# Optimization experiments

Hardware: AMD Instinct MI355X
Metric: run time of the kernel (lower is better)

The kernel has to match this reference:

```python
import jax, jax.numpy as jnp
import numpy as np

D = 1024        # embed_size
F = 4096        # ffn_dim
E = 8           # n_experts
K = 2           # top_k_experts
NS = 1          # n_shared
T = 8192        # tokens


def setup_inputs() -> dict:
    key = jax.random.key(0)
    ks = jax.random.split(key, 12)
    s = lambda *sh: 1.0 / np.sqrt(sh[-2] if len(sh) > 1 else sh[-1])
    inp = {
        "x": jax.random.normal(ks[0], (T, D), jnp.float32),
        "gate_w": jax.random.normal(ks[1], (D, E), jnp.float32) * (1.0 / np.sqrt(D)),
        "gate_b": jnp.zeros((E,), jnp.float32),
        "shared_w1": jax.random.normal(ks[2], (NS, D, 2 * F), jnp.float32) * (1.0 / np.sqrt(D)),
        "shared_b1": jnp.zeros((NS, 2 * F), jnp.float32),
        "shared_w2": jax.random.normal(ks[3], (NS, F, D), jnp.float32) * (1.0 / np.sqrt(F)),
        "shared_b2": jnp.zeros((NS, D), jnp.float32),
        "routed_w1": jax.random.normal(ks[4], (E, D, 2 * F), jnp.float32) * (1.0 / np.sqrt(D)),
        "routed_b1": jnp.zeros((E, 2 * F), jnp.float32),
        "routed_w2": jax.random.normal(ks[5], (E, F, D), jnp.float32) * (1.0 / np.sqrt(F)),
        "routed_b2": jnp.zeros((E, D), jnp.float32),
    }
    return inp


def _expert(x, w1, b1, w2, b2):
    # SwiGLU FFN: w2( silu(a) * b ) where [a, b] = chunk(x @ w1 + b1)
    h = x @ w1 + b1                      # [T, 2F]
    a, b = jnp.split(h, 2, axis=-1)      # [T, F] each
    return (jax.nn.silu(a) * b) @ w2 + b2  # [T, D]


def reference(x, gate_w, gate_b, shared_w1, shared_b1, shared_w2, shared_b2,
              routed_w1, routed_b1, routed_w2, routed_b2):
    # shared experts (always active)
    shared_out = jnp.zeros_like(x)
    for i in range(NS):
        shared_out = shared_out + _expert(x, shared_w1[i], shared_b1[i], shared_w2[i], shared_b2[i])

    # softmax gating + top-k selection
    logits = x @ gate_w + gate_b                      # [T, E]
    probs = jax.nn.softmax(logits, axis=-1)
    topk_probs, topk_idx = jax.lax.top_k(probs, K)    # [T, K]

    # per-token combine weight for each expert: sum_k p_k * 1[idx_k == e]
    one_hot = jax.nn.one_hot(topk_idx, E, dtype=x.dtype)        # [T, K, E]
    combine = jnp.einsum("tk,tke->te", topk_probs, one_hot)     # [T, E]

    # dispatch/combine: dense per-expert FFN, weighted by combine (zero off-route)
    routed_out = jnp.zeros_like(x)
    for e in range(E):
        y = _expert(x, routed_w1[e], routed_b1[e], routed_w2[e], routed_b2[e])
        routed_out = routed_out + y * combine[:, e:e + 1]

    return shared_out + routed_out
```

## Files before the change

kernel.cpp:

```cpp
#include <hip/hip_runtime.h>

#define TOK   8192
#define DD    1024
#define FF    4096
#define EE    8
#define TWOF  8192
#define NSLOT 16384
#define PADT  17408

typedef unsigned short u16;
typedef float  f32x16 __attribute__((ext_vector_type(16)));
typedef __bf16 bf16x8 __attribute__((ext_vector_type(8)));

__device__ __forceinline__ u16 f2b(float f) {
  unsigned u = __builtin_bit_cast(unsigned, f);
  u += 0x7fffu + ((u >> 16) & 1u);
  return (u16)(u >> 16);
}

__device__ __forceinline__ void ldslds16(const void* g, void* l) {
  __builtin_amdgcn_global_load_lds((const __attribute__((address_space(1))) void*)g,
                                   (__attribute__((address_space(3))) void*)l, 16, 0, 0);
}

__global__ void gate_kernel(const float* __restrict__ x, const float* __restrict__ gw,
                            const float* __restrict__ gb, int* __restrict__ counts,
                            int* __restrict__ eidx, int* __restrict__ epos,
                            float* __restrict__ ew) {
  const int wave = threadIdx.x >> 6, lane = threadIdx.x & 63;
  const int t = blockIdx.x * 4 + wave;
  float acc[EE] = {0,0,0,0,0,0,0,0};
  const float* xr = x + (size_t)t * DD;
  for (int d = lane; d < DD; d += 64) {
    float xv = xr[d];
    const float* g = gw + (size_t)d * EE;
#pragma unroll
    for (int e = 0; e < EE; ++e) acc[e] += xv * g[e];
  }
#pragma unroll
  for (int e = 0; e < EE; ++e)
#pragma unroll
    for (int off = 32; off > 0; off >>= 1) acc[e] += __shfl_down(acc[e], off);
  if (lane == 0) {
    float l[EE];
#pragma unroll
    for (int e = 0; e < EE; ++e) l[e] = acc[e] + gb[e];
    int i0 = 0;
    for (int e = 1; e < EE; ++e) if (l[e] > l[i0]) i0 = e;
    int i1 = (i0 == 0) ? 1 : 0;
    for (int e = 0; e < EE; ++e) { if (e == i0) continue; if (l[e] > l[i1]) i1 = e; }
    float m = l[0];
    for (int e = 1; e < EE; ++e) m = fmaxf(m, l[e]);
    float s = 0.f, p[EE];
    for (int e = 0; e < EE; ++e) { p[e] = __expf(l[e] - m); s += p[e]; }
    float w0 = p[i0] / s, w1 = p[i1] / s;
    int p0 = atomicAdd(&counts[i0], 1);
    int p1 = atomicAdd(&counts[i1], 1);
    eidx[2*t] = i0; eidx[2*t+1] = i1;
    epos[2*t] = p0; epos[2*t+1] = p1;
    ew[2*t] = w0;  ew[2*t+1] = w1;
  }
}

__global__ void setup_kernel(const int* __restrict__ counts, int* __restrict__ meta) {
  if (threadIdx.x == 0 && blockIdx.x == 0) {
    int s = 0, tm = 0;
    for (int e = 0; e < EE; ++e) {
      meta[e] = s;
      meta[8 + e] = tm;
      s  += (counts[e] + 127) & ~127;
      tm += (counts[e] + 127) >> 7;
    }
    meta[16] = tm;
  }
}

__global__ void slot_kernel(const int* __restrict__ eidx, const int* __restrict__ epos,
                            const float* __restrict__ ew, const int* __restrict__ meta,
                            int* __restrict__ s2t, float* __restrict__ swt,
                            int* __restrict__ t2s) {
  int i = blockIdx.x * 256 + threadIdx.x;
  int e = eidx[i];
  int slot = meta[e] + epos[i];
  s2t[slot] = i >> 1;
  swt[slot] = ew[i];
  t2s[i] = slot;
}

__global__ void cvtx_kernel(const float* __restrict__ x, u16* __restrict__ xb) {
  int i = blockIdx.x * 256 + threadIdx.x;
  float4 v = ((const float4*)x)[i];
  unsigned lo = (unsigned)f2b(v.x) | ((unsigned)f2b(v.y) << 16);
  unsigned hi = (unsigned)f2b(v.z) | ((unsigned)f2b(v.w) << 16);
  ((uint2*)xb)[i] = make_uint2(lo, hi);
}

__global__ void gather_kernel(const u16* __restrict__ xb, const int* __restrict__ s2t,
                              u16* __restrict__ xg) {
  int i = blockIdx.x * 256 + threadIdx.x;
  int row = i >> 7, c = i & 127;
  int tok = s2t[row];
  ((int4*)xg)[(size_t)row * 128 + c] = ((const int4*)xb)[(size_t)tok * 128 + c];
}

__global__ void wt_kernel(const float* __restrict__ srcS, const float* __restrict__ srcR,
                          u16* __restrict__ dst, int K, int N, int permute) {
  __shared__ float tile[32][33];
  const int seg = blockIdx.z;
  const float* src = (seg == 0) ? srcS : srcR + (size_t)(seg - 1) * K * N;
  const int pc0 = blockIdx.x * 32, k0 = blockIdx.y * 32;
  const int tid = threadIdx.x;
  {
    int kk = tid >> 3, j4 = (tid & 7) << 2;
    const float* srow = src + (size_t)(k0 + kk) * N;
#pragma unroll
    for (int q = 0; q < 4; ++q) {
      int n = pc0 + j4 + q;
      int oc = permute ? (((n >> 6) << 5) + (n & 31) + ((n & 32) ? FF : 0)) : n;
      tile[kk][j4 + q] = srow[oc];
    }
  }
  __syncthreads();
  {
    int pp = tid >> 3, kq = (tid & 7) << 2;
    u16* drow = dst + (size_t)seg * N * K + (size_t)(pc0 + pp) * K + k0 + kq;
#pragma unroll
    for (int q = 0; q < 4; ++q) drow[q] = f2b(tile[kq + q][pp]);
  }
}


__device__ __forceinline__ void kloop32(int niter,
    const char* a0, const char* a1, const char* a2, const char* a3,
    const char* b0, const char* b1, const char* b2, const char* b3,
    u16* As, u16* Bs, int tid, f32x16 (&acc)[2][2]) {
  const int lane = tid & 63, l31 = lane & 31, kg = (lane >> 5) * 16;
  const int wid = tid >> 6, wm = wid >> 1, wn = wid & 1;
  const int C = (l31 & 7) << 4;
  const char* rA[4]; const char* rB[4];
#pragma unroll
  for (int ks = 0; ks < 4; ++ks) {
    const int o = (ks * 32 + kg) ^ C;
    rA[ks] = (const char*)As + (wm * 64 + l31) * 128 + o;
    rB[ks] = (const char*)Bs + (wn * 64 + l31) * 128 + o;
  }
  for (int it = 0; it < niter; ++it) {
    const long long kb = (long long)it * 128;
    ldslds16(a0 + kb, As + tid * 8);
    ldslds16(a1 + kb, As + 2048 + tid * 8);
    ldslds16(a2 + kb, As + 4096 + tid * 8);
    ldslds16(a3 + kb, As + 6144 + tid * 8);
    ldslds16(b0 + kb, Bs + tid * 8);
    ldslds16(b1 + kb, Bs + 2048 + tid * 8);
    ldslds16(b2 + kb, Bs + 4096 + tid * 8);
    ldslds16(b3 + kb, Bs + 6144 + tid * 8);
    __syncthreads();
#pragma unroll
    for (int ks = 0; ks < 4; ++ks) {
      bf16x8 af0 = *(const bf16x8*)(rA[ks]);
      bf16x8 af1 = *(const bf16x8*)(rA[ks] + 4096);
      bf16x8 bq0 = *(const bf16x8*)(rB[ks]);
      bf16x8 bq1 = *(const bf16x8*)(rB[ks] + 4096);
      acc[0][0] = __builtin_amdgcn_mfma_f32_32x32x16_bf16(af0, bq0, acc[0][0], 0, 0, 0);
      acc[0][1] = __builtin_amdgcn_mfma_f32_32x32x16_bf16(af0, bq1, acc[0][1], 0, 0, 0);
      acc[1][0] = __builtin_amdgcn_mfma_f32_32x32x16_bf16(af1, bq0, acc[1][0], 0, 0, 0);
      acc[1][1] = __builtin_amdgcn_mfma_f32_32x32x16_bf16(af1, bq1, acc[1][1], 0, 0, 0);
    }
    __syncthreads();
  }
}

__device__ __forceinline__ bool seg_map(int g, const int* __restrict__ counts,
                                        const int* __restrict__ meta,
                                        int& seg, int& tm, int& rowstart, int& rows) {
  if (g < 64) { seg = 0; tm = g; rowstart = 0; rows = TOK; return true; }
  int gr = g - 64;
  if (gr >= meta[16]) return false;
  int e = 0;
  while (gr >= meta[8 + e + 1]) ++e;
  seg = e + 1; tm = gr - meta[8 + e];
  rowstart = meta[e]; rows = counts[e];
  return true;
}

__global__ __launch_bounds__(256, 4)
void gemm1_kernel(const u16* __restrict__ xb, const u16* __restrict__ xg,
                  const u16* __restrict__ w1t, const float* __restrict__ sb1,
                  const float* __restrict__ rb1, const int* __restrict__ counts,
                  const int* __restrict__ meta, u16* __restrict__ hs) {
  __shared__ __align__(16) u16 As[128 * 64];
  __shared__ __align__(16) u16 Bs[128 * 64];
  const int lin = blockIdx.x + 64 * blockIdx.y;
  const int tn = (lin & 7) * 8 + ((lin >> 3) & 7);
  const int g = lin >> 6;
  int seg, tm, rowstart, rows;
  if (!seg_map(g, counts, meta, seg, tm, rowstart, rows)) return;
  const u16* A = (seg == 0) ? xb : xg;
  const int hsbase = (seg == 0) ? 0 : TOK + rowstart;
  const int tid = threadIdx.x, lane = tid & 63, wid = tid >> 6;
  const int wm = wid >> 1, wn = wid & 1;

  const int srow = tid >> 3;
  const int scol = ((tid & 7) * 16) ^ ((srow & 7) << 4);
  const char* Ac = (const char*)A;
  const char* Bc = (const char*)(w1t + (size_t)seg * TWOF * DD);
  const char* a[4]; const char* b[4];
#pragma unroll
  for (int r = 0; r < 4; ++r) {
    int rg = rowstart + tm * 128 + r * 32 + srow;
    a[r] = Ac + (size_t)rg * (DD * 2) + scol;
    b[r] = Bc + (size_t)(tn * 128 + r * 32 + srow) * (DD * 2) + scol;
  }

  f32x16 acc[2][2] = {};
  kloop32(DD / 64, a[0], a[1], a[2], a[3], b[0], b[1], b[2], b[3],
          As, Bs, tid, acc);

  const int l31 = lane & 31, lg = lane >> 5;
  const int rlim = rows - tm * 128;
  const float* b1 = (seg == 0) ? sb1 : rb1 + (size_t)(seg - 1) * TWOF;
  const int f = (tn * 2 + wn) * 32 + l31;
  const float ba = b1[f], bb = b1[FF + f];
  u16* hbase = hs + (size_t)(hsbase + tm * 128) * FF;
#pragma unroll
  for (int mi = 0; mi < 2; ++mi)
#pragma unroll
    for (int reg = 0; reg < 16; ++reg) {
      int lr = wm * 64 + mi * 32 + (reg & 3) + 8 * (reg >> 2) + 4 * lg;
      if (lr < rlim) {
        float av = acc[mi][0][reg] + ba;
        float bv = acc[mi][1][reg] + bb;
        float sv = av / (1.0f + __expf(-av)) * bv;
        hbase[(size_t)lr * FF + f] = f2b(sv);
      }
    }
}

__global__ __launch_bounds__(256, 4)
void gemm2_kernel(const u16* __restrict__ hs, const u16* __restrict__ w2t,
                  const float* __restrict__ sb2, const float* __restrict__ rb2,
                  const int* __restrict__ counts, const int* __restrict__ meta,
                  float* __restrict__ yo) {
  __shared__ __align__(16) u16 As[128 * 64];
  __shared__ __align__(16) u16 Bs[128 * 64];
  const int tn = blockIdx.x;
  const int g = blockIdx.y;
  int seg, tm, rowstart, rows;
  if (!seg_map(g, counts, meta, seg, tm, rowstart, rows)) return;
  const int hrow0 = (seg == 0) ? 0 : TOK + rowstart;
  const int tid = threadIdx.x, lane = tid & 63, wid = tid >> 6;
  const int wm = wid >> 1, wn = wid & 1;

  const int srow = tid >> 3;
  const int scol = ((tid & 7) * 16) ^ ((srow & 7) << 4);
  const char* Ac = (const char*)hs;
  const char* Bc = (const char*)(w2t + (size_t)seg * DD * FF);
  const char* a[4]; const char* b[4];
#pragma unroll
  for (int r = 0; r < 4; ++r) {
    a[r] = Ac + (size_t)(hrow0 + tm * 128 + r * 32 + srow) * (FF * 2) + scol;
    b[r] = Bc + (size_t)(tn * 128 + r * 32 + srow) * (FF * 2) + scol;
  }

  f32x16 acc[2][2] = {};
  kloop32(FF / 64, a[0], a[1], a[2], a[3], b[0], b[1], b[2], b[3],
          As, Bs, tid, acc);

  const int l31 = lane & 31, lg = lane >> 5;
  const int rlim = rows - tm * 128;
  const float* b2 = (seg == 0) ? sb2 : rb2 + (size_t)(seg - 1) * DD;
  const int c0 = tn * 128 + wn * 64 + l31;
  const float bias0 = b2[c0], bias1 = b2[c0 + 32];
  float* ybase = yo + (size_t)(hrow0 + tm * 128) * DD;
#pragma unroll
  for (int mi = 0; mi < 2; ++mi)
#pragma unroll
    for (int reg = 0; reg < 16; ++reg) {
      int lr = wm * 64 + mi * 32 + (reg & 3) + 8 * (reg >> 2) + 4 * lg;
      if (lr < rlim) {
        float* orow = ybase + (size_t)lr * DD;
        orow[c0]      = acc[mi][0][reg] + bias0;
        orow[c0 + 32] = acc[mi][1][reg] + bias1;
      }
    }
}

__global__ void combine_kernel(const float* __restrict__ yo, const int* __restrict__ t2s,
                               const float* __restrict__ ew, float* __restrict__ out) {
  const int t = blockIdx.x, d = threadIdx.x;
  const float4 a  = ((const float4*)(yo + (size_t)t * DD))[d];
  const int s0 = t2s[2*t], s1 = t2s[2*t+1];
  const float w0 = ew[2*t], w1 = ew[2*t+1];
  const float4 r0 = ((const float4*)(yo + (size_t)(TOK + s0) * DD))[d];
  const float4 r1 = ((const float4*)(yo + (size_t)(TOK + s1) * DD))[d];
  float4 r;
  r.x = a.x + w0 * r0.x + w1 * r1.x;
  r.y = a.y + w0 * r0.y + w1 * r1.y;
  r.z = a.z + w0 * r0.z + w1 * r1.z;
  r.w = a.w + w0 * r0.w + w1 * r1.w;
  ((float4*)(out + (size_t)t * DD))[d] = r;
}

extern "C" void kernel_launch(void* const* d_in, const int* in_sizes, int n_in,
                              void* d_out, int out_size, void* d_ws, size_t ws_size,
                              hipStream_t stream) {
  const float* x   = (const float*)d_in[0];
  const float* gw  = (const float*)d_in[1];
  const float* gb  = (const float*)d_in[2];
  const float* sw1 = (const float*)d_in[3];
  const float* sb1 = (const float*)d_in[4];
  const float* sw2 = (const float*)d_in[5];
  const float* sb2 = (const float*)d_in[6];
  const float* rw1 = (const float*)d_in[7];
  const float* rb1 = (const float*)d_in[8];
  const float* rw2 = (const float*)d_in[9];
  const float* rb2 = (const float*)d_in[10];
  float* out = (float*)d_out;

  char* p = (char*)d_ws;
  auto alloc = [&](size_t bytes) { char* r = p; p += (bytes + 255) & ~(size_t)255; return r; };
  int*   counts = (int*)alloc(EE * 4);
  int*   meta   = (int*)alloc(17 * 4);
  int*   eidx   = (int*)alloc((size_t)2 * TOK * 4);
  int*   epos   = (int*)alloc((size_t)2 * TOK * 4);
  float* ew     = (float*)alloc((size_t)2 * TOK * 4);
  int*   s2t    = (int*)alloc((size_t)PADT * 4);
  float* swt    = (float*)alloc((size_t)PADT * 4);
  int*   t2s    = (int*)alloc((size_t)2 * TOK * 4);
  u16*   xb     = (u16*)alloc((size_t)TOK * DD * 2);
  u16*   xg     = (u16*)alloc((size_t)PADT * DD * 2);
  u16*   w1t    = (u16*)alloc((size_t)9 * TWOF * DD * 2);
  u16*   w2t    = (u16*)alloc((size_t)9 * DD * FF * 2);
  u16*   hs     = (u16*)alloc((size_t)(TOK + PADT + 128) * FF * 2);
  float* yo     = (float*)w1t;

  hipMemsetAsync(counts, 0, EE * 4, stream);
  hipMemsetAsync(s2t, 0, (size_t)PADT * 4, stream);
  gate_kernel<<<TOK / 4, 256, 0, stream>>>(x, gw, gb, counts, eidx, epos, ew);
  setup_kernel<<<1, 64, 0, stream>>>(counts, meta);
  slot_kernel<<<(2 * TOK) / 256, 256, 0, stream>>>(eidx, epos, ew, meta, s2t, swt, t2s);
  cvtx_kernel<<<(TOK * DD / 4) / 256, 256, 0, stream>>>(x, xb);
  gather_kernel<<<PADT / 2, 256, 0, stream>>>(xb, s2t, xg);
  wt_kernel<<<dim3(TWOF / 32, DD / 32, 9), 256, 0, stream>>>(sw1, rw1, w1t, DD, TWOF, 1);
  wt_kernel<<<dim3(DD / 32, FF / 32, 9), 256, 0, stream>>>(sw2, rw2, w2t, FF, DD, 0);
  gemm1_kernel<<<dim3(64, 199), 256, 0, stream>>>(xb, xg, w1t, sb1, rb1, counts, meta, hs);
  gemm2_kernel<<<dim3(8, 199), 256, 0, stream>>>(hs, w2t, sb2, rb2, counts, meta, yo);
  combine_kernel<<<TOK, 256, 0, stream>>>(yo, t2s, ew, out);
}
```

Before: 1.112 ms.

## Fuse bf16 cast into gating, drop gather/setup kernels, widen weight transpose tiles

The bf16 conversion of x now happens inside the gate kernel, and the separate cast kernel is removed. The gather kernel is replaced by indirect row addressing through s2t inside gemm1. The setup/meta kernel is removed, so slot offsets and segment mapping are recomputed from counts on each use. The weight-transpose kernel moves to 64x64 tiles with 16-byte packed bf16 stores, and the grid y dimension changes from 199 to 200. This cuts several launches and a full gathered-activation copy, at the cost of indirect, less coalesced A loads in gemm1 and a little repeated prefix-sum work.

```diff
diff --git a/kernel.cpp b/kernel.cpp
--- a/kernel.cpp
+++ b/kernel.cpp
@@ -26,13 +26,15 @@
 __global__ void gate_kernel(const float* __restrict__ x, const float* __restrict__ gw,
                             const float* __restrict__ gb, int* __restrict__ counts,
                             int* __restrict__ eidx, int* __restrict__ epos,
-                            float* __restrict__ ew) {
+                            float* __restrict__ ew, u16* __restrict__ xb) {
   const int wave = threadIdx.x >> 6, lane = threadIdx.x & 63;
   const int t = blockIdx.x * 4 + wave;
   float acc[EE] = {0,0,0,0,0,0,0,0};
   const float* xr = x + (size_t)t * DD;
+  u16* xbr = xb + (size_t)t * DD;
   for (int d = lane; d < DD; d += 64) {
     float xv = xr[d];
+    xbr[d] = f2b(xv);
     const float* g = gw + (size_t)d * EE;
 #pragma unroll
     for (int e = 0; e < EE; ++e) acc[e] += xv * g[e];
@@ -62,70 +64,51 @@
   }
 }
 
-__global__ void setup_kernel(const int* __restrict__ counts, int* __restrict__ meta) {
-  if (threadIdx.x == 0 && blockIdx.x == 0) {
-    int s = 0, tm = 0;
-    for (int e = 0; e < EE; ++e) {
-      meta[e] = s;
-      meta[8 + e] = tm;
-      s  += (counts[e] + 127) & ~127;
-      tm += (counts[e] + 127) >> 7;
-    }
-    meta[16] = tm;
-  }
-}
-
 __global__ void slot_kernel(const int* __restrict__ eidx, const int* __restrict__ epos,
-                            const float* __restrict__ ew, const int* __restrict__ meta,
+                            const float* __restrict__ ew, const int* __restrict__ counts,
                             int* __restrict__ s2t, float* __restrict__ swt,
                             int* __restrict__ t2s) {
   int i = blockIdx.x * 256 + threadIdx.x;
   int e = eidx[i];
-  int slot = meta[e] + epos[i];
+  int off = 0;
+  for (int j = 0; j < e; ++j) off += (counts[j] + 127) & ~127;
+  int slot = off + epos[i];
   s2t[slot] = i >> 1;
   swt[slot] = ew[i];
   t2s[i] = slot;
 }
 
-__global__ void cvtx_kernel(const float* __restrict__ x, u16* __restrict__ xb) {
-  int i = blockIdx.x * 256 + threadIdx.x;
-  float4 v = ((const float4*)x)[i];
-  unsigned lo = (unsigned)f2b(v.x) | ((unsigned)f2b(v.y) << 16);
-  unsigned hi = (unsigned)f2b(v.z) | ((unsigned)f2b(v.w) << 16);
-  ((uint2*)xb)[i] = make_uint2(lo, hi);
-}
-
-__global__ void gather_kernel(const u16* __restrict__ xb, const int* __restrict__ s2t,
-                              u16* __restrict__ xg) {
-  int i = blockIdx.x * 256 + threadIdx.x;
-  int row = i >> 7, c = i & 127;
-  int tok = s2t[row];
-  ((int4*)xg)[(size_t)row * 128 + c] = ((const int4*)xb)[(size_t)tok * 128 + c];
-}
-
 __global__ void wt_kernel(const float* __restrict__ srcS, const float* __restrict__ srcR,
                           u16* __restrict__ dst, int K, int N, int permute) {
-  __shared__ float tile[32][33];
+  __shared__ float tile[64][65];
   const int seg = blockIdx.z;
   const float* src = (seg == 0) ? srcS : srcR + (size_t)(seg - 1) * K * N;
-  const int pc0 = blockIdx.x * 32, k0 = blockIdx.y * 32;
+  const int pc0 = blockIdx.x * 64, k0 = blockIdx.y * 64;
   const int tid = threadIdx.x;
   {
-    int kk = tid >> 3, j4 = (tid & 7) << 2;
+    int kk = tid >> 2, j0 = (tid & 3) * 16;
     const float* srow = src + (size_t)(k0 + kk) * N;
 #pragma unroll
-    for (int q = 0; q < 4; ++q) {
-      int n = pc0 + j4 + q;
+    for (int q = 0; q < 16; ++q) {
+      int n = pc0 + j0 + q;
       int oc = permute ? (((n >> 6) << 5) + (n & 31) + ((n & 32) ? FF : 0)) : n;
-      tile[kk][j4 + q] = srow[oc];
+      tile[kk][j0 + q] = srow[oc];
     }
   }
   __syncthreads();
   {
-    int pp = tid >> 3, kq = (tid & 7) << 2;
-    u16* drow = dst + (size_t)seg * N * K + (size_t)(pc0 + pp) * K + k0 + kq;
-#pragma unroll
-    for (int q = 0; q < 4; ++q) drow[q] = f2b(tile[kq + q][pp]);
+    int pp = tid & 63;
+    u16* drow = dst + (size_t)seg * N * K + (size_t)(pc0 + pp) * K + k0;
+#pragma unroll
+    for (int h = 0; h < 2; ++h) {
+      int kq = (tid >> 6) * 16 + h * 8;
+      uint4 v;
+      unsigned* pv = (unsigned*)&v;
+#pragma unroll
+      for (int q = 0; q < 4; ++q)
+        pv[q] = (unsigned)f2b(tile[kq + 2*q][pp]) | ((unsigned)f2b(tile[kq + 2*q + 1][pp]) << 16);
+      *(uint4*)(drow + kq) = v;
+    }
   }
 }
 
@@ -171,43 +154,44 @@
 }
 
 __device__ __forceinline__ bool seg_map(int g, const int* __restrict__ counts,
-                                        const int* __restrict__ meta,
                                         int& seg, int& tm, int& rowstart, int& rows) {
   if (g < 64) { seg = 0; tm = g; rowstart = 0; rows = TOK; return true; }
-  int gr = g - 64;
-  if (gr >= meta[16]) return false;
-  int e = 0;
-  while (gr >= meta[8 + e + 1]) ++e;
-  seg = e + 1; tm = gr - meta[8 + e];
-  rowstart = meta[e]; rows = counts[e];
-  return true;
+  int gr = g - 64, off = 0;
+  for (int e = 0; e < EE; ++e) {
+    int c = counts[e];
+    int nb = (c + 127) >> 7;
+    if (gr < nb) { seg = e + 1; tm = gr; rowstart = off; rows = c; return true; }
+    gr -= nb;
+    off += (c + 127) & ~127;
+  }
+  return false;
 }
 
 __global__ __launch_bounds__(256, 4)
-void gemm1_kernel(const u16* __restrict__ xb, const u16* __restrict__ xg,
+void gemm1_kernel(const u16* __restrict__ xb, const int* __restrict__ s2t,
                   const u16* __restrict__ w1t, const float* __restrict__ sb1,
                   const float* __restrict__ rb1, const int* __restrict__ counts,
-                  const int* __restrict__ meta, u16* __restrict__ hs) {
+                  u16* __restrict__ hs) {
   __shared__ __align__(16) u16 As[128 * 64];
   __shared__ __align__(16) u16 Bs[128 * 64];
   const int lin = blockIdx.x + 64 * blockIdx.y;
   const int tn = (lin & 7) * 8 + ((lin >> 3) & 7);
   const int g = lin >> 6;
   int seg, tm, rowstart, rows;
-  if (!seg_map(g, counts, meta, seg, tm, rowstart, rows)) return;
-  const u16* A = (seg == 0) ? xb : xg;
+  if (!seg_map(g, counts, seg, tm, rowstart, rows)) return;
   const int hsbase = (seg == 0) ? 0 : TOK + rowstart;
   const int tid = threadIdx.x, lane = tid & 63, wid = tid >> 6;
   const int wm = wid >> 1, wn = wid & 1;
 
   const int srow = tid >> 3;
   const int scol = ((tid & 7) * 16) ^ ((srow & 7) << 4);
-  const char* Ac = (const char*)A;
+  const char* Ac = (const char*)xb;
   const char* Bc = (const char*)(w1t + (size_t)seg * TWOF * DD);
   const char* a[4]; const char* b[4];
 #pragma unroll
   for (int r = 0; r < 4; ++r) {
-    int rg = rowstart + tm * 128 + r * 32 + srow;
+    int rbase = tm * 128 + r * 32 + srow;
+    int rg = (seg == 0) ? rbase : s2t[rowstart + rbase];
     a[r] = Ac + (size_t)rg * (DD * 2) + scol;
     b[r] = Bc + (size_t)(tn * 128 + r * 32 + srow) * (DD * 2) + scol;
   }
@@ -239,14 +223,13 @@
 __global__ __launch_bounds__(256, 4)
 void gemm2_kernel(const u16* __restrict__ hs, const u16* __restrict__ w2t,
                   const float* __restrict__ sb2, const float* __restrict__ rb2,
-                  const int* __restrict__ counts, const int* __restrict__ meta,
-                  float* __restrict__ yo) {
+                  const int* __restrict__ counts, float* __restrict__ yo) {
   __shared__ __align__(16) u16 As[128 * 64];
   __shared__ __align__(16) u16 Bs[128 * 64];
   const int tn = blockIdx.x;
   const int g = blockIdx.y;
   int seg, tm, rowstart, rows;
-  if (!seg_map(g, counts, meta, seg, tm, rowstart, rows)) return;
+  if (!seg_map(g, counts, seg, tm, rowstart, rows)) return;
   const int hrow0 = (seg == 0) ? 0 : TOK + rowstart;
   const int tid = threadIdx.x, lane = tid & 63, wid = tid >> 6;
   const int wm = wid >> 1, wn = wid & 1;
@@ -320,7 +303,6 @@
   char* p = (char*)d_ws;
   auto alloc = [&](size_t bytes) { char* r = p; p += (bytes + 255) & ~(size_t)255; return r; };
   int*   counts = (int*)alloc(EE * 4);
-  int*   meta   = (int*)alloc(17 * 4);
   int*   eidx   = (int*)alloc((size_t)2 * TOK * 4);
   int*   epos   = (int*)alloc((size_t)2 * TOK * 4);
   float* ew     = (float*)alloc((size_t)2 * TOK * 4);
@@ -328,7 +310,6 @@
   float* swt    = (float*)alloc((size_t)PADT * 4);
   int*   t2s    = (int*)alloc((size_t)2 * TOK * 4);
   u16*   xb     = (u16*)alloc((size_t)TOK * DD * 2);
-  u16*   xg     = (u16*)alloc((size_t)PADT * DD * 2);
   u16*   w1t    = (u16*)alloc((size_t)9 * TWOF * DD * 2);
   u16*   w2t    = (u16*)alloc((size_t)9 * DD * FF * 2);
   u16*   hs     = (u16*)alloc((size_t)(TOK + PADT + 128) * FF * 2);
@@ -336,14 +317,11 @@
 
   hipMemsetAsync(counts, 0, EE * 4, stream);
   hipMemsetAsync(s2t, 0, (size_t)PADT * 4, stream);
-  gate_kernel<<<TOK / 4, 256, 0, stream>>>(x, gw, gb, counts, eidx, epos, ew);
-  setup_kernel<<<1, 64, 0, stream>>>(counts, meta);
-  slot_kernel<<<(2 * TOK) / 256, 256, 0, stream>>>(eidx, epos, ew, meta, s2t, swt, t2s);
-  cvtx_kernel<<<(TOK * DD / 4) / 256, 256, 0, stream>>>(x, xb);
-  gather_kernel<<<PADT / 2, 256, 0, stream>>>(xb, s2t, xg);
-  wt_kernel<<<dim3(TWOF / 32, DD / 32, 9), 256, 0, stream>>>(sw1, rw1, w1t, DD, TWOF, 1);
-  wt_kernel<<<dim3(DD / 32, FF / 32, 9), 256, 0, stream>>>(sw2, rw2, w2t, FF, DD, 0);
-  gemm1_kernel<<<dim3(64, 199), 256, 0, stream>>>(xb, xg, w1t, sb1, rb1, counts, meta, hs);
-  gemm2_kernel<<<dim3(8, 199), 256, 0, stream>>>(hs, w2t, sb2, rb2, counts, meta, yo);
+  gate_kernel<<<TOK / 4, 256, 0, stream>>>(x, gw, gb, counts, eidx, epos, ew, xb);
+  slot_kernel<<<(2 * TOK) / 256, 256, 0, stream>>>(eidx, epos, ew, counts, s2t, swt, t2s);
+  wt_kernel<<<dim3(TWOF / 64, DD / 64, 9), 256, 0, stream>>>(sw1, rw1, w1t, DD, TWOF, 1);
+  wt_kernel<<<dim3(DD / 64, FF / 64, 9), 256, 0, stream>>>(sw2, rw2, w2t, FF, DD, 0);
+  gemm1_kernel<<<dim3(64, 200), 256, 0, stream>>>(xb, s2t, w1t, sb1, rb1, counts, hs);
+  gemm2_kernel<<<dim3(8, 200), 256, 0, stream>>>(hs, w2t, sb2, rb2, counts, yo);
   combine_kernel<<<TOK, 256, 0, stream>>>(yo, t2s, ew, out);
 }
```

Measured after the change: 1.229 ms. +10.5%, slower.
